# Optimization experiments

Hardware: AMD Instinct MI355X
Metric: run time of the kernel (lower is better)

## Reference

```python
import jax, jax.numpy as jnp
import numpy as np

B, L, D = 32, 4096, 64
TOP_K = 2
KS = 25            # AvgPool1d kernel_size
PAD = (KS - 1) // 2
LN_EPS = 1e-5


def setup_inputs() -> dict:
    key = jax.random.key(0)
    ks = jax.random.split(key, 8)
    s = lambda fan_in: 1.0 / np.sqrt(fan_in)
    return {
        "x": jax.random.normal(ks[0], (B, L, 1), dtype=jnp.float32),
        "embed_w": jax.random.normal(ks[1], (1, D), dtype=jnp.float32) * s(1),
        "embed_b": jnp.zeros((D,), jnp.float32),
        "q_w": jax.random.normal(ks[2], (D, D), dtype=jnp.float32) * s(D),
        "q_b": jnp.zeros((D,), jnp.float32),
        "k_w": jax.random.normal(ks[3], (D, D), dtype=jnp.float32) * s(D),
        "k_b": jnp.zeros((D,), jnp.float32),
        "v_w": jax.random.normal(ks[4], (D, D), dtype=jnp.float32) * s(D),
        "v_b": jnp.zeros((D,), jnp.float32),
        "ln_g": jnp.ones((D,), jnp.float32),
        "ln_b": jnp.zeros((D,), jnp.float32),
        "fc_w": jax.random.normal(ks[5], (L * D, 1), dtype=jnp.float32) * s(L * D),
        "fc_b": jnp.zeros((1,), jnp.float32),
    }


def _auto_correlation(h, q_w, q_b, k_w, k_b, v_w, v_b):
    Q = h @ q_w + q_b          # (B, L, D)
    K = h @ k_w + k_b
    V = h @ v_w + v_b
    q_fft = jnp.fft.rfft(Q, axis=1)
    k_fft = jnp.fft.rfft(K, axis=1)
    corr = jnp.fft.irfft(q_fft * jnp.conj(k_fft), n=L, axis=1)  # (B, L, D)
    mean_corr = corr.mean(axis=-1)                               # (B, L)
    topk_vals, topk_idx = jax.lax.top_k(mean_corr, TOP_K)        # (B, K)
    weights = jax.nn.softmax(topk_vals, axis=-1)                 # (B, K)
    # torch.roll(V[b], shift=lag): out[i] = V[(i - lag) mod L]
    idx = (jnp.arange(L)[None, None, :] - topk_idx[:, :, None]) % L   # (B, K, L)
    Vg = jnp.take_along_axis(V[:, None, :, :], idx[..., None], axis=2)  # (B, K, L, D)
    return jnp.einsum("bk,bkld->bld", weights, Vg)


def _moving_avg(h):
    # AvgPool1d(kernel=KS, stride=1, pad=PAD, count_include_pad=True) over time axis
    hp = jnp.pad(h, ((0, 0), (PAD, PAD), (0, 0)))
    cs = jnp.pad(jnp.cumsum(hp, axis=1), ((0, 0), (1, 0), (0, 0)))
    return (cs[:, KS:, :] - cs[:, :-KS, :]) / KS   # (B, L, D)


def reference(x, embed_w, embed_b, q_w, q_b, k_w, k_b, v_w, v_b,
              ln_g, ln_b, fc_w, fc_b):
    h = x @ embed_w + embed_b                       # (B, L, D)
    ac = _auto_correlation(h, q_w, q_b, k_w, k_b, v_w, v_b)
    z = h + ac
    mu = z.mean(axis=-1, keepdims=True)
    var = z.var(axis=-1, keepdims=True)
    hn = (z - mu) * jax.lax.rsqrt(var + LN_EPS) * ln_g + ln_b
    trend = _moving_avg(hn)
    seasonal = hn - trend
    return seasonal.reshape(B, L * D) @ fc_w + fc_b  # (B, 1)
```

## Files before the change

kernel.cpp:

```cpp
#include <hip/hip_runtime.h>
#include <math.h>

#define LQ 4096
#define DQ 64
#define BQ 32
#define KSQ 25
#define PADQ 12
#define LN_EPS 1e-5f

#define NT 8
#define TCH (LQ / NT)
#define NAC (BQ * 2 * NT)

#define WS_PART 16384

__device__ __forceinline__ float wave_sum64(float v) {
    for (int o = 32; o > 0; o >>= 1) v += __shfl_xor(v, o, 64);
    return v;
}

__device__ __forceinline__ bool ac_better(float v, int i, float v2, int i2) {
    return (v > v2) || (v == v2 && i < i2);
}

__global__ void ac_stage1_kernel(const float* __restrict__ x,
                                 const float* __restrict__ fc_w,
                                 const float* __restrict__ ln_g,
                                 const float* __restrict__ ln_b,
                                 const float* __restrict__ embed_w,
                                 const float* __restrict__ embed_b,
                                 const float* __restrict__ v_w,
                                 const float* __restrict__ v_b,
                                 float* __restrict__ ws) {
    __shared__ float smem[2048];
    int tid = threadIdx.x;

    if (blockIdx.x < NAC) {
        float* sA = smem;
        float* sB = smem + TCH;
        int b = blockIdx.x & 31;
        int y = (blockIdx.x >> 5) & 1;
        int z = blockIdx.x >> 6;
        int lagbase = y << 10;
        int t0 = z * TCH;
        const float* xb = x + (size_t)b * LQ;

        for (int i = tid; i < TCH; i += 256) sA[i] = xb[t0 + i];
        int start = t0 - lagbase - 1023;
        for (int j = tid; j < TCH + 1024; j += 256)
            sB[j] = xb[(start + j + LQ) & (LQ - 1)];
        __syncthreads();

        const float4* sA4 = (const float4*)sA;
        const float4* sB4 = (const float4*)sB;
        int base = 255 - tid;
        float4 w0 = sB4[base];
        float a0 = 0.f, a1 = 0.f, a2 = 0.f, a3 = 0.f;
#pragma unroll 4
        for (int c = 0; c < TCH / 4; ++c) {
            float4 w1 = sB4[base + c + 1];
            float4 xa = sA4[c];
            a0 = fmaf(xa.x, w0.w, a0); a1 = fmaf(xa.x, w0.z, a1); a2 = fmaf(xa.x, w0.y, a2); a3 = fmaf(xa.x, w0.x, a3);
            a0 = fmaf(xa.y, w1.x, a0); a1 = fmaf(xa.y, w0.w, a1); a2 = fmaf(xa.y, w0.z, a2); a3 = fmaf(xa.y, w0.y, a3);
            a0 = fmaf(xa.z, w1.y, a0); a1 = fmaf(xa.z, w1.x, a1); a2 = fmaf(xa.z, w0.w, a2); a3 = fmaf(xa.z, w0.z, a3);
            a0 = fmaf(xa.w, w1.z, a0); a1 = fmaf(xa.w, w1.y, a1); a2 = fmaf(xa.w, w1.x, a2); a3 = fmaf(xa.w, w0.w, a3);
            w0 = w1;
        }
        float4* part4 = (float4*)(ws + WS_PART);
        part4[((size_t)(z * BQ + b) * 512) + (y * 256) + tid] =
            make_float4(a0, a1, a2, a3);
    } else {
        float* Hu = smem;
        float* Hv = smem + 280;
        float* Hw = smem + 560;
        float* Hb = smem + 840;
        float* su = smem + 1120;
        float* sv = smem + 1184;
        float* sw = smem + 1248;
        float* sb = smem + 1312;

        if (tid < DQ) {
            int d = tid;
            float Av = 0.f, Cv = 0.f;
#pragma unroll 8
            for (int e = 0; e < DQ; ++e) {
                float vw = v_w[e * DQ + d];
                Av = fmaf(embed_w[e], vw, Av);
                Cv = fmaf(embed_b[e], vw, Cv);
            }
            Cv += v_b[d];
            float cx = embed_w[d];
            float cs = Av;
            float cc = embed_b[d] + Cv;
            const float invD = 1.f / (float)DQ;
            float mx = wave_sum64(cx) * invD;
            float ms = wave_sum64(cs) * invD;
            float mc = wave_sum64(cc) * invD;
            float g = ln_g[d];
            su[d] = (cx - mx) * g;
            sv[d] = (cs - ms) * g;
            sw[d] = (cc - mc) * g;
            sb[d] = ln_b[d];
        }
        __syncthreads();

        int lbase = (blockIdx.x - NAC) * 256;
        for (int i = tid; i < 256 + 2 * PADQ; i += 256) {
            int l = lbase - PADQ + i;
            float fu = 0.f, fv = 0.f, fw = 0.f, fb = 0.f;
            if (l >= 0 && l < LQ) {
                const float4* fc = (const float4*)(fc_w + (size_t)l * DQ);
#pragma unroll
                for (int d4 = 0; d4 < DQ / 4; ++d4) {
                    float4 f = fc[d4];
                    int d = d4 * 4;
                    fu = fmaf(su[d], f.x, fu); fu = fmaf(su[d+1], f.y, fu); fu = fmaf(su[d+2], f.z, fu); fu = fmaf(su[d+3], f.w, fu);
                    fv = fmaf(sv[d], f.x, fv); fv = fmaf(sv[d+1], f.y, fv); fv = fmaf(sv[d+2], f.z, fv); fv = fmaf(sv[d+3], f.w, fv);
                    fw = fmaf(sw[d], f.x, fw); fw = fmaf(sw[d+1], f.y, fw); fw = fmaf(sw[d+2], f.z, fw); fw = fmaf(sw[d+3], f.w, fw);
                    fb = fmaf(sb[d], f.x, fb); fb = fmaf(sb[d+1], f.y, fb); fb = fmaf(sb[d+2], f.z, fb); fb = fmaf(sb[d+3], f.w, fb);
                }
            }
            Hu[i] = fu; Hv[i] = fv; Hw[i] = fw; Hb[i] = fb;
        }
        __syncthreads();

        int l = lbase + tid;
        int i = tid + PADQ;
        float Gu = 0.f, Gv = 0.f, Gw = 0.f;
#pragma unroll
        for (int k = -PADQ; k <= PADQ; ++k) {
            Gu += Hu[i + k]; Gv += Hv[i + k]; Gw += Hw[i + k];
        }
        int lo = l - PADQ; if (lo < 0) lo = 0;
        int hi = l + PADQ; if (hi > LQ - 1) hi = LQ - 1;
        const float inv = 1.f / (float)KSQ;
        float cnt = (float)(hi - lo + 1);
        ws[l]          = Hu[i] - Gu * inv;
        ws[LQ + l]     = Hv[i] - Gv * inv;
        ws[2 * LQ + l] = Hw[i] - Gw * inv;
        ws[3 * LQ + l] = (1.f - cnt * inv) * Hb[i];
    }
}

__global__ void __launch_bounds__(1024)
ac_final_kernel(const float* __restrict__ x,
                const float* __restrict__ embed_w, const float* __restrict__ embed_b,
                const float* __restrict__ q_w, const float* __restrict__ q_b,
                const float* __restrict__ k_w, const float* __restrict__ k_b,
                const float* __restrict__ v_w, const float* __restrict__ v_b,
                const float* __restrict__ fc_b,
                const float* __restrict__ ws,
                float* __restrict__ out) {
    __shared__ float4 xs4_[LQ / 4];
    __shared__ float scal[16];
    __shared__ float red[32];
    __shared__ float tv0[16], tv1[16];
    __shared__ int   ti0[16], ti1[16];
    float* xs_ = (float*)xs4_;

    int b = blockIdx.x;
    int tid = threadIdx.x;
    int wv = tid >> 6;
    const float* xb = x + (size_t)b * LQ;

    xs4_[tid] = ((const float4*)xb)[tid];

    if (tid < DQ) {
        int d = tid;
        float Aq = 0.f, Cq = 0.f, Ak = 0.f, Ck = 0.f, Av = 0.f, Cv = 0.f;
#pragma unroll 8
        for (int e = 0; e < DQ; ++e) {
            float we = embed_w[e], be = embed_b[e];
            float qw = q_w[e * DQ + d], kw = k_w[e * DQ + d], vw = v_w[e * DQ + d];
            Aq = fmaf(we, qw, Aq); Cq = fmaf(be, qw, Cq);
            Ak = fmaf(we, kw, Ak); Ck = fmaf(be, kw, Ck);
            Av = fmaf(we, vw, Av); Cv = fmaf(be, vw, Cv);
        }
        Cq += q_b[d]; Ck += k_b[d]; Cv += v_b[d];
        float cx = embed_w[d];
        float cs = Av;
        float cc = embed_b[d] + Cv;
        const float invD = 1.f / (float)DQ;
        float mx = wave_sum64(cx) * invD;
        float ms = wave_sum64(cs) * invD;
        float mc = wave_sum64(cc) * invD;
        float cxp = cx - mx, csp = cs - ms, ccp = cc - mc;
        float Mxx = wave_sum64(cxp * cxp) * invD;
        float Mss = wave_sum64(csp * csp) * invD;
        float Mcc = wave_sum64(ccp * ccp) * invD;
        float Mxs = wave_sum64(cxp * csp) * invD;
        float Mxc = wave_sum64(cxp * ccp) * invD;
        float Msc = wave_sum64(csp * ccp) * invD;
        float alpha = wave_sum64(Aq * Ak) * invD;
        float beta  = wave_sum64(Aq * Ck + Ak * Cq) * invD;
        float gamma = wave_sum64(Cq * Ck) * ((float)LQ * invD);
        if (d == 0) {
            scal[2] = alpha; scal[3] = beta; scal[4] = gamma;
            scal[5] = Mxx; scal[6] = Mss; scal[7] = Mcc;
            scal[8] = Mxs; scal[9] = Mxc; scal[10] = Msc;
        }
    }
    __syncthreads();

    {
        float sx = 0.f, r2k = 0.f;
#pragma unroll
        for (int k = 0; k < 4; ++k) {
            int t = tid + k * 1024;
            float v = xs_[t];
            sx  += v;
            r2k += v * xs_[(t + 2048) & (LQ - 1)];
        }
        sx  = wave_sum64(sx);
        r2k = wave_sum64(r2k);
        if ((tid & 63) == 0) { red[wv] = sx; red[16 + wv] = r2k; }
    }
    __syncthreads();
    if (tid == 0) {
        float sx = 0.f, r2k = 0.f;
#pragma unroll
        for (int w = 0; w < 16; ++w) { sx += red[w]; r2k += red[16 + w]; }
        scal[0] = sx; scal[1] = r2k;
        scal[11] = fmaf(scal[3], sx, scal[4]);
    }
    __syncthreads();

    {
        float alpha = scal[2], cbase = scal[11];
        float v0 = -3.0e38f, v1 = -3.0e38f;
        int i0 = 1 << 30, i1 = 1 << 30;
        const float* part = ws + WS_PART;
#pragma unroll
        for (int k = 0; k < 2; ++k) {
            int lag = tid + k * 1024;
            float R = 0.f;
#pragma unroll
            for (int z = 0; z < NT; ++z)
                R += part[((size_t)(z * BQ + b) * 2048) + lag];
            float v = fmaf(alpha, R, cbase);
            if (ac_better(v, lag, v0, i0)) { v1 = v0; i1 = i0; v0 = v; i0 = lag; }
            else if (ac_better(v, lag, v1, i1)) { v1 = v; i1 = lag; }
            int mir = (LQ - lag) & (LQ - 1);
            if (mir != lag) {
                if (ac_better(v, mir, v0, i0)) { v1 = v0; i1 = i0; v0 = v; i0 = mir; }
                else if (ac_better(v, mir, v1, i1)) { v1 = v; i1 = mir; }
            }
        }
        for (int o = 32; o > 0; o >>= 1) {
            float u0 = __shfl_xor(v0, o, 64); int j0 = __shfl_xor(i0, o, 64);
            float u1 = __shfl_xor(v1, o, 64); int j1 = __shfl_xor(i1, o, 64);
            if (ac_better(u0, j0, v0, i0)) {
                if (ac_better(v0, i0, u1, j1)) { v1 = v0; i1 = i0; }
                else                           { v1 = u1; i1 = j1; }
                v0 = u0; i0 = j0;
            } else if (ac_better(u0, j0, v1, i1)) { v1 = u0; i1 = j0; }
        }
        if ((tid & 63) == 0) { tv0[wv] = v0; ti0[wv] = i0; tv1[wv] = v1; ti1[wv] = i1; }
    }
    __syncthreads();
    if (tid == 0) {
        float v0 = tv0[0], v1 = tv1[0];
        int i0 = ti0[0], i1 = ti1[0];
#pragma unroll
        for (int w = 1; w < 16; ++w) {
            float u0 = tv0[w], u1 = tv1[w];
            int j0 = ti0[w], j1 = ti1[w];
            if (ac_better(u0, j0, v0, i0)) {
                if (ac_better(v0, i0, u1, j1)) { v1 = v0; i1 = i0; }
                else                           { v1 = u1; i1 = j1; }
                v0 = u0; i0 = j0;
            } else if (ac_better(u0, j0, v1, i1)) { v1 = u0; i1 = j0; }
        }
        float v2k = fmaf(scal[2], scal[1], scal[11]);
        if (ac_better(v2k, 2048, v0, i0)) {
            if (ac_better(v0, i0, v1, i1)) { v1 = v0; i1 = i0; }
            v0 = v2k; i0 = 2048;
        } else if (ac_better(v2k, 2048, v1, i1)) { v1 = v2k; i1 = 2048; }
        float w0 = 1.f / (1.f + expf(v1 - v0));
        scal[12] = (float)i0; scal[13] = (float)i1;
        scal[14] = w0; scal[15] = 1.f - w0;
    }
    __syncthreads();

    {
        int lag0 = (int)scal[12], lag1 = (int)scal[13];
        float w0 = scal[14], w1 = scal[15];
        float Mxx = scal[5], Mss = scal[6], Mcc = scal[7];
        float Mxs = scal[8], Mxc = scal[9], Msc = scal[10];
        const float* Fpu = ws;
        const float* Fpv = ws + LQ;
        const float* Fpw = ws + 2 * LQ;
        const float* FBp = ws + 3 * LQ;
        float acc = 0.f;
#pragma unroll
        for (int k = 0; k < 4; ++k) {
            int l = tid + k * 1024;
            float xv = xs_[l];
            float xsv = w0 * xs_[(l - lag0) & (LQ - 1)] + w1 * xs_[(l - lag1) & (LQ - 1)];
            float var = xv * xv * Mxx + xsv * xsv * Mss + Mcc
                      + 2.f * xv * xsv * Mxs + 2.f * xv * Mxc + 2.f * xsv * Msc;
            float r = rsqrtf(var + LN_EPS);
            acc += (xv * r) * Fpu[l] + (xsv * r) * Fpv[l] + r * Fpw[l] + FBp[l];
        }
        acc = wave_sum64(acc);
        if ((tid & 63) == 0) red[wv] = acc;
    }
    __syncthreads();
    if (tid == 0) {
        float s = 0.f;
#pragma unroll
        for (int w = 0; w < 16; ++w) s += red[w];
        out[b] = s + fc_b[0];
    }
}

extern "C" void kernel_launch(void* const* d_in, const int* in_sizes, int n_in,
                              void* d_out, int out_size, void* d_ws, size_t ws_size,
                              hipStream_t stream) {
    const float* x       = (const float*)d_in[0];
    const float* embed_w = (const float*)d_in[1];
    const float* embed_b = (const float*)d_in[2];
    const float* q_w     = (const float*)d_in[3];
    const float* q_b     = (const float*)d_in[4];
    const float* k_w     = (const float*)d_in[5];
    const float* k_b     = (const float*)d_in[6];
    const float* v_w     = (const float*)d_in[7];
    const float* v_b     = (const float*)d_in[8];
    const float* ln_g    = (const float*)d_in[9];
    const float* ln_b    = (const float*)d_in[10];
    const float* fc_w    = (const float*)d_in[11];
    const float* fc_b    = (const float*)d_in[12];
    float* out = (float*)d_out;
    float* ws  = (float*)d_ws;

    ac_stage1_kernel<<<NAC + 16, 256, 0, stream>>>(x, fc_w, ln_g, ln_b,
                                                   embed_w, embed_b, v_w, v_b, ws);
    ac_final_kernel<<<BQ, 1024, 0, stream>>>(x, embed_w, embed_b, q_w, q_b,
                                             k_w, k_b, v_w, v_b, fc_b, ws, out);
}
```

Before: 116.6 us.

## Compute 8 lags per thread in correlation and move per-batch scalars to stage one

The circular autocorrelation stage now assigns 8 consecutive lags per thread instead of 4. Each thread covers all 2048 lags in one block per (batch, time chunk), which halves the block count and reuses each loaded x element across more FMAs. The weight-derived scalar constants and the per-batch sums (sum of x and lag-2048 correlation) move out of the final kernel into extra stage-one blocks written to workspace. This shortens the serial prologue of the final kernel. The cost is more register pressure and a larger shared-memory window per correlation block, plus fewer correlation blocks for parallelism.

```diff
diff --git a/kernel.cpp b/kernel.cpp
--- a/kernel.cpp
+++ b/kernel.cpp
@@ -10,9 +10,14 @@
 
 #define NT 8
 #define TCH (LQ / NT)
-#define NAC (BQ * 2 * NT)
+#define NAC (BQ * NT)
+#define NFP 16
+#define NPB 16
+#define NBLK (NAC + NFP + NPB)
 
 #define WS_PART 16384
+#define WS_SCAL (WS_PART + NT * BQ * 2048)
+#define WS_SB   (WS_SCAL + 16)
 
 __device__ __forceinline__ float wave_sum64(float v) {
     for (int o = 32; o > 0; o >>= 1) v += __shfl_xor(v, o, 64);
@@ -23,53 +28,64 @@
     return (v > v2) || (v == v2 && i < i2);
 }
 
-__global__ void ac_stage1_kernel(const float* __restrict__ x,
-                                 const float* __restrict__ fc_w,
-                                 const float* __restrict__ ln_g,
-                                 const float* __restrict__ ln_b,
-                                 const float* __restrict__ embed_w,
-                                 const float* __restrict__ embed_b,
-                                 const float* __restrict__ v_w,
-                                 const float* __restrict__ v_b,
-                                 float* __restrict__ ws) {
-    __shared__ float smem[2048];
+__device__ __forceinline__ void top2_upd(float v, int i,
+                                         float& v0, int& i0, float& v1, int& i1) {
+    if (ac_better(v, i, v0, i0)) { v1 = v0; i1 = i0; v0 = v; i0 = i; }
+    else if (ac_better(v, i, v1, i1)) { v1 = v; i1 = i; }
+}
+
+__global__ void __launch_bounds__(256)
+ac_stage1_kernel(const float* __restrict__ x,
+                 const float* __restrict__ fc_w,
+                 const float* __restrict__ ln_g, const float* __restrict__ ln_b,
+                 const float* __restrict__ embed_w, const float* __restrict__ embed_b,
+                 const float* __restrict__ q_w, const float* __restrict__ q_b,
+                 const float* __restrict__ k_w, const float* __restrict__ k_b,
+                 const float* __restrict__ v_w, const float* __restrict__ v_b,
+                 float* __restrict__ ws) {
+    __shared__ float smem[3072];
     int tid = threadIdx.x;
-
-    if (blockIdx.x < NAC) {
+    int blk = blockIdx.x;
+
+    if (blk < NAC) {
         float* sA = smem;
         float* sB = smem + TCH;
-        int b = blockIdx.x & 31;
-        int y = (blockIdx.x >> 5) & 1;
-        int z = blockIdx.x >> 6;
-        int lagbase = y << 10;
+        int b = blk & 31;
+        int z = blk >> 5;
         int t0 = z * TCH;
         const float* xb = x + (size_t)b * LQ;
 
         for (int i = tid; i < TCH; i += 256) sA[i] = xb[t0 + i];
-        int start = t0 - lagbase - 1023;
-        for (int j = tid; j < TCH + 1024; j += 256)
+        int start = t0 - 2047;
+        for (int j = tid; j < TCH + 2048; j += 256)
             sB[j] = xb[(start + j + LQ) & (LQ - 1)];
         __syncthreads();
 
         const float4* sA4 = (const float4*)sA;
         const float4* sB4 = (const float4*)sB;
-        int base = 255 - tid;
-        float4 w0 = sB4[base];
+        int B0 = 510 - 2 * tid;
+        float4 w0 = sB4[B0];
+        float4 w1 = sB4[B0 + 1];
         float a0 = 0.f, a1 = 0.f, a2 = 0.f, a3 = 0.f;
+        float a4 = 0.f, a5 = 0.f, a6 = 0.f, a7 = 0.f;
 #pragma unroll 4
-        for (int c = 0; c < TCH / 4; ++c) {
-            float4 w1 = sB4[base + c + 1];
-            float4 xa = sA4[c];
-            a0 = fmaf(xa.x, w0.w, a0); a1 = fmaf(xa.x, w0.z, a1); a2 = fmaf(xa.x, w0.y, a2); a3 = fmaf(xa.x, w0.x, a3);
-            a0 = fmaf(xa.y, w1.x, a0); a1 = fmaf(xa.y, w0.w, a1); a2 = fmaf(xa.y, w0.z, a2); a3 = fmaf(xa.y, w0.y, a3);
-            a0 = fmaf(xa.z, w1.y, a0); a1 = fmaf(xa.z, w1.x, a1); a2 = fmaf(xa.z, w0.w, a2); a3 = fmaf(xa.z, w0.z, a3);
-            a0 = fmaf(xa.w, w1.z, a0); a1 = fmaf(xa.w, w1.y, a1); a2 = fmaf(xa.w, w1.x, a2); a3 = fmaf(xa.w, w0.w, a3);
-            w0 = w1;
-        }
-        float4* part4 = (float4*)(ws + WS_PART);
-        part4[((size_t)(z * BQ + b) * 512) + (y * 256) + tid] =
-            make_float4(a0, a1, a2, a3);
-    } else {
+        for (int c4 = 0; c4 < TCH / 4; ++c4) {
+            float4 w2 = sB4[B0 + c4 + 2];
+            float4 xa = sA4[c4];
+            a7 = fmaf(xa.x, w0.x, a7); a7 = fmaf(xa.y, w0.y, a7); a7 = fmaf(xa.z, w0.z, a7); a7 = fmaf(xa.w, w0.w, a7);
+            a6 = fmaf(xa.x, w0.y, a6); a6 = fmaf(xa.y, w0.z, a6); a6 = fmaf(xa.z, w0.w, a6); a6 = fmaf(xa.w, w1.x, a6);
+            a5 = fmaf(xa.x, w0.z, a5); a5 = fmaf(xa.y, w0.w, a5); a5 = fmaf(xa.z, w1.x, a5); a5 = fmaf(xa.w, w1.y, a5);
+            a4 = fmaf(xa.x, w0.w, a4); a4 = fmaf(xa.y, w1.x, a4); a4 = fmaf(xa.z, w1.y, a4); a4 = fmaf(xa.w, w1.z, a4);
+            a3 = fmaf(xa.x, w1.x, a3); a3 = fmaf(xa.y, w1.y, a3); a3 = fmaf(xa.z, w1.z, a3); a3 = fmaf(xa.w, w1.w, a3);
+            a2 = fmaf(xa.x, w1.y, a2); a2 = fmaf(xa.y, w1.z, a2); a2 = fmaf(xa.z, w1.w, a2); a2 = fmaf(xa.w, w2.x, a2);
+            a1 = fmaf(xa.x, w1.z, a1); a1 = fmaf(xa.y, w1.w, a1); a1 = fmaf(xa.z, w2.x, a1); a1 = fmaf(xa.w, w2.y, a1);
+            a0 = fmaf(xa.x, w1.w, a0); a0 = fmaf(xa.y, w2.x, a0); a0 = fmaf(xa.z, w2.y, a0); a0 = fmaf(xa.w, w2.z, a0);
+            w0 = w1; w1 = w2;
+        }
+        float4* part4 = (float4*)(ws + WS_PART + (size_t)(z * BQ + b) * 2048);
+        part4[2 * tid]     = make_float4(a0, a1, a2, a3);
+        part4[2 * tid + 1] = make_float4(a4, a5, a6, a7);
+    } else if (blk < NAC + NFP) {
         float* Hu = smem;
         float* Hv = smem + 280;
         float* Hw = smem + 560;
@@ -104,7 +120,7 @@
         }
         __syncthreads();
 
-        int lbase = (blockIdx.x - NAC) * 256;
+        int lbase = (blk - NAC) * 256;
         for (int i = tid; i < 256 + 2 * PADQ; i += 256) {
             int l = lbase - PADQ + i;
             float fu = 0.f, fv = 0.f, fw = 0.f, fb = 0.f;
@@ -139,21 +155,77 @@
         ws[LQ + l]     = Hv[i] - Gv * inv;
         ws[2 * LQ + l] = Hw[i] - Gw * inv;
         ws[3 * LQ + l] = (1.f - cnt * inv) * Hb[i];
+    } else {
+        int i = blk - (NAC + NFP);
+#pragma unroll
+        for (int bb = 0; bb < 2; ++bb) {
+            int b = i * 2 + bb;
+            const float* xb = x + (size_t)b * LQ;
+            float sx = 0.f, r2k = 0.f;
+#pragma unroll
+            for (int k = 0; k < LQ / 256; ++k) {
+                int t = tid + k * 256;
+                float v = xb[t];
+                sx  += v;
+                r2k += v * xb[(t + 2048) & (LQ - 1)];
+            }
+            sx  = wave_sum64(sx);
+            r2k = wave_sum64(r2k);
+            int wv = tid >> 6;
+            if ((tid & 63) == 0) { smem[wv] = sx; smem[8 + wv] = r2k; }
+            __syncthreads();
+            if (tid == 0) {
+                ws[WS_SB + b]      = smem[0] + smem[1] + smem[2] + smem[3];
+                ws[WS_SB + BQ + b] = smem[8] + smem[9] + smem[10] + smem[11];
+            }
+            __syncthreads();
+        }
+        if (i == 0 && tid < DQ) {
+            int d = tid;
+            float Aq = 0.f, Cq = 0.f, Ak = 0.f, Ck = 0.f, Av = 0.f, Cv = 0.f;
+#pragma unroll 8
+            for (int e = 0; e < DQ; ++e) {
+                float we = embed_w[e], be = embed_b[e];
+                float qw = q_w[e * DQ + d], kw = k_w[e * DQ + d], vw = v_w[e * DQ + d];
+                Aq = fmaf(we, qw, Aq); Cq = fmaf(be, qw, Cq);
+                Ak = fmaf(we, kw, Ak); Ck = fmaf(be, kw, Ck);
+                Av = fmaf(we, vw, Av); Cv = fmaf(be, vw, Cv);
+            }
+            Cq += q_b[d]; Ck += k_b[d]; Cv += v_b[d];
+            float cx = embed_w[d];
+            float cs = Av;
+            float cc = embed_b[d] + Cv;
+            const float invD = 1.f / (float)DQ;
+            float mx = wave_sum64(cx) * invD;
+            float ms = wave_sum64(cs) * invD;
+            float mc = wave_sum64(cc) * invD;
+            float cxp = cx - mx, csp = cs - ms, ccp = cc - mc;
+            float Mxx = wave_sum64(cxp * cxp) * invD;
+            float Mss = wave_sum64(csp * csp) * invD;
+            float Mcc = wave_sum64(ccp * ccp) * invD;
+            float Mxs = wave_sum64(cxp * csp) * invD;
+            float Mxc = wave_sum64(cxp * ccp) * invD;
+            float Msc = wave_sum64(csp * ccp) * invD;
+            float alpha = wave_sum64(Aq * Ak) * invD;
+            float beta  = wave_sum64(Aq * Ck + Ak * Cq) * invD;
+            float gamma = wave_sum64(Cq * Ck) * ((float)LQ * invD);
+            if (d == 0) {
+                ws[WS_SCAL + 0] = alpha; ws[WS_SCAL + 1] = beta; ws[WS_SCAL + 2] = gamma;
+                ws[WS_SCAL + 3] = Mxx; ws[WS_SCAL + 4] = Mss; ws[WS_SCAL + 5] = Mcc;
+                ws[WS_SCAL + 6] = Mxs; ws[WS_SCAL + 7] = Mxc; ws[WS_SCAL + 8] = Msc;
+            }
+        }
     }
 }
 
 __global__ void __launch_bounds__(1024)
 ac_final_kernel(const float* __restrict__ x,
-                const float* __restrict__ embed_w, const float* __restrict__ embed_b,
-                const float* __restrict__ q_w, const float* __restrict__ q_b,
-                const float* __restrict__ k_w, const float* __restrict__ k_b,
-                const float* __restrict__ v_w, const float* __restrict__ v_b,
                 const float* __restrict__ fc_b,
                 const float* __restrict__ ws,
                 float* __restrict__ out) {
     __shared__ float4 xs4_[LQ / 4];
-    __shared__ float scal[16];
-    __shared__ float red[32];
+    __shared__ float scal[32];
+    __shared__ float red[16];
     __shared__ float tv0[16], tv1[16];
     __shared__ int   ti0[16], ti1[16];
     float* xs_ = (float*)xs4_;
@@ -165,68 +237,13 @@
 
     xs4_[tid] = ((const float4*)xb)[tid];
 
-    if (tid < DQ) {
-        int d = tid;
-        float Aq = 0.f, Cq = 0.f, Ak = 0.f, Ck = 0.f, Av = 0.f, Cv = 0.f;
-#pragma unroll 8
-        for (int e = 0; e < DQ; ++e) {
-            float we = embed_w[e], be = embed_b[e];
-            float qw = q_w[e * DQ + d], kw = k_w[e * DQ + d], vw = v_w[e * DQ + d];
-            Aq = fmaf(we, qw, Aq); Cq = fmaf(be, qw, Cq);
-            Ak = fmaf(we, kw, Ak); Ck = fmaf(be, kw, Ck);
-            Av = fmaf(we, vw, Av); Cv = fmaf(be, vw, Cv);
-        }
-        Cq += q_b[d]; Ck += k_b[d]; Cv += v_b[d];
-        float cx = embed_w[d];
-        float cs = Av;
-        float cc = embed_b[d] + Cv;
-        const float invD = 1.f / (float)DQ;
-        float mx = wave_sum64(cx) * invD;
-        float ms = wave_sum64(cs) * invD;
-        float mc = wave_sum64(cc) * invD;
-        float cxp = cx - mx, csp = cs - ms, ccp = cc - mc;
-        float Mxx = wave_sum64(cxp * cxp) * invD;
-        float Mss = wave_sum64(csp * csp) * invD;
-        float Mcc = wave_sum64(ccp * ccp) * invD;
-        float Mxs = wave_sum64(cxp * csp) * invD;
-        float Mxc = wave_sum64(cxp * ccp) * invD;
-        float Msc = wave_sum64(csp * ccp) * invD;
-        float alpha = wave_sum64(Aq * Ak) * invD;
-        float beta  = wave_sum64(Aq * Ck + Ak * Cq) * invD;
-        float gamma = wave_sum64(Cq * Ck) * ((float)LQ * invD);
-        if (d == 0) {
-            scal[2] = alpha; scal[3] = beta; scal[4] = gamma;
-            scal[5] = Mxx; scal[6] = Mss; scal[7] = Mcc;
-            scal[8] = Mxs; scal[9] = Mxc; scal[10] = Msc;
-        }
-    }
-    __syncthreads();
+    float alpha = ws[WS_SCAL + 0], beta = ws[WS_SCAL + 1], gamma = ws[WS_SCAL + 2];
+    float Mxx = ws[WS_SCAL + 3], Mss = ws[WS_SCAL + 4], Mcc = ws[WS_SCAL + 5];
+    float Mxs = ws[WS_SCAL + 6], Mxc = ws[WS_SCAL + 7], Msc = ws[WS_SCAL + 8];
+    float Sxb = ws[WS_SB + b], R2k = ws[WS_SB + BQ + b];
+    float cbase = fmaf(beta, Sxb, gamma);
 
     {
-        float sx = 0.f, r2k = 0.f;
-#pragma unroll
-        for (int k = 0; k < 4; ++k) {
-            int t = tid + k * 1024;
-            float v = xs_[t];
-            sx  += v;
-            r2k += v * xs_[(t + 2048) & (LQ - 1)];
-        }
-        sx  = wave_sum64(sx);
-        r2k = wave_sum64(r2k);
-        if ((tid & 63) == 0) { red[wv] = sx; red[16 + wv] = r2k; }
-    }
-    __syncthreads();
-    if (tid == 0) {
-        float sx = 0.f, r2k = 0.f;
-#pragma unroll
-        for (int w = 0; w < 16; ++w) { sx += red[w]; r2k += red[16 + w]; }
-        scal[0] = sx; scal[1] = r2k;
-        scal[11] = fmaf(scal[3], sx, scal[4]);
-    }
-    __syncthreads();
-
-    {
-        float alpha = scal[2], cbase = scal[11];
         float v0 = -3.0e38f, v1 = -3.0e38f;
         int i0 = 1 << 30, i1 = 1 << 30;
         const float* part = ws + WS_PART;
@@ -238,13 +255,9 @@
             for (int z = 0; z < NT; ++z)
                 R += part[((size_t)(z * BQ + b) * 2048) + lag];
             float v = fmaf(alpha, R, cbase);
-            if (ac_better(v, lag, v0, i0)) { v1 = v0; i1 = i0; v0 = v; i0 = lag; }
-            else if (ac_better(v, lag, v1, i1)) { v1 = v; i1 = lag; }
+            top2_upd(v, lag, v0, i0, v1, i1);
             int mir = (LQ - lag) & (LQ - 1);
-            if (mir != lag) {
-                if (ac_better(v, mir, v0, i0)) { v1 = v0; i1 = i0; v0 = v; i0 = mir; }
-                else if (ac_better(v, mir, v1, i1)) { v1 = v; i1 = mir; }
-            }
+            if (mir != lag) top2_upd(v, mir, v0, i0, v1, i1);
         }
         for (int o = 32; o > 0; o >>= 1) {
             float u0 = __shfl_xor(v0, o, 64); int j0 = __shfl_xor(i0, o, 64);
@@ -271,22 +284,20 @@
                 v0 = u0; i0 = j0;
             } else if (ac_better(u0, j0, v1, i1)) { v1 = u0; i1 = j0; }
         }
-        float v2k = fmaf(scal[2], scal[1], scal[11]);
+        float v2k = fmaf(alpha, R2k, cbase);
         if (ac_better(v2k, 2048, v0, i0)) {
             if (ac_better(v0, i0, v1, i1)) { v1 = v0; i1 = i0; }
             v0 = v2k; i0 = 2048;
         } else if (ac_better(v2k, 2048, v1, i1)) { v1 = v2k; i1 = 2048; }
         float w0 = 1.f / (1.f + expf(v1 - v0));
-        scal[12] = (float)i0; scal[13] = (float)i1;
-        scal[14] = w0; scal[15] = 1.f - w0;
+        scal[0] = (float)i0; scal[1] = (float)i1;
+        scal[2] = w0; scal[3] = 1.f - w0;
     }
     __syncthreads();
 
     {
-        int lag0 = (int)scal[12], lag1 = (int)scal[13];
-        float w0 = scal[14], w1 = scal[15];
-        float Mxx = scal[5], Mss = scal[6], Mcc = scal[7];
-        float Mxs = scal[8], Mxc = scal[9], Msc = scal[10];
+        int lag0 = (int)scal[0], lag1 = (int)scal[1];
+        float w0 = scal[2], w1 = scal[3];
         const float* Fpu = ws;
         const float* Fpv = ws + LQ;
         const float* Fpw = ws + 2 * LQ;
@@ -333,8 +344,8 @@
     float* out = (float*)d_out;
     float* ws  = (float*)d_ws;
 
-    ac_stage1_kernel<<<NAC + 16, 256, 0, stream>>>(x, fc_w, ln_g, ln_b,
-                                                   embed_w, embed_b, v_w, v_b, ws);
-    ac_final_kernel<<<BQ, 1024, 0, stream>>>(x, embed_w, embed_b, q_w, q_b,
-                                             k_w, k_b, v_w, v_b, fc_b, ws, out);
-}
+    ac_stage1_kernel<<<NBLK, 256, 0, stream>>>(x, fc_w, ln_g, ln_b,
+                                               embed_w, embed_b,
+                                               q_w, q_b, k_w, k_b, v_w, v_b, ws);
+    ac_final_kernel<<<BQ, 1024, 0, stream>>>(x, fc_b, ws, out);
+}
```

New measurement: 111.6 us, median of 2. 1.05x faster.
